# Optimization experiments

Hardware: AMD Instinct MI355X
Metric: run time of the kernel (lower is better)

## Reference

```python
import jax, jax.numpy as jnp
from jax import lax
import numpy as np

D_MODEL = 512
D_INNER = 1024   # expand=2 * d_model
D_STATE = 16
D_CONV = 4
DT_RANK = 32     # ceil(d_model/16)
B_SZ = 2
SEQ = 8192


def setup_inputs() -> dict:
    key = jax.random.key(0)
    ks = jax.random.split(key, 20)
    def n(k, shape, s=0.02):
        return jax.random.normal(k, shape, jnp.float32) * s
    inp = {
        "hidden_states": jax.random.normal(ks[0], (B_SZ, SEQ, D_MODEL), jnp.float32),
        "in_proj_w": n(ks[1], (2 * D_INNER, D_MODEL)),
        "out_proj_w": n(ks[2], (D_MODEL, D_INNER)),
    }
    for i, sfx in enumerate(["f", "r"]):
        b = 3 + i * 7
        inp[f"conv_w_{sfx}"] = n(ks[b], (D_INNER, 1, D_CONV), 0.1)
        inp[f"conv_b_{sfx}"] = n(ks[b + 1], (D_INNER,), 0.1)
        inp[f"xproj_w_{sfx}"] = n(ks[b + 2], (DT_RANK + 2 * D_STATE, D_INNER))
        inp[f"dtproj_w_{sfx}"] = n(ks[b + 3], (D_INNER, DT_RANK), 0.1)
        # softplus-inverse of dt_init ~0.01 (Mamba-style dt bias init)
        inp[f"dtproj_b_{sfx}"] = jnp.log(jnp.expm1(jnp.full((D_INNER,), 0.01, jnp.float32)))
        inp[f"A_log_{sfx}"] = jnp.log(jnp.tile(jnp.arange(1, D_STATE + 1, dtype=jnp.float32), (D_INNER, 1)))
        inp[f"D_{sfx}"] = jnp.ones((D_INNER,), jnp.float32)
    return inp


def _mamba(u, in_w, out_w, conv_w, conv_b, xproj_w, dt_w, dt_b, A_log, D_skip):
    # u: (B, L, D_MODEL)
    B, L, _ = u.shape
    xz = jnp.einsum('bld,ed->ble', u, in_w)          # (B, L, 2*D_INNER)
    x, z = jnp.split(xz, 2, axis=-1)
    # depthwise causal conv1d over time
    xt = lax.conv_general_dilated(
        x.transpose(0, 2, 1), conv_w, (1,), [(D_CONV - 1, 0)],
        dimension_numbers=('NCH', 'OIH', 'NCH'), feature_group_count=D_INNER)
    x = jax.nn.silu(xt.transpose(0, 2, 1) + conv_b)   # (B, L, D_INNER)
    # input-dependent dt, B, C
    xdbl = jnp.einsum('ble,fe->blf', x, xproj_w)      # (B, L, DT_RANK + 2*D_STATE)
    dt = xdbl[..., :DT_RANK]
    Bm = xdbl[..., DT_RANK:DT_RANK + D_STATE]         # (B, L, N)
    Cm = xdbl[..., DT_RANK + D_STATE:]                # (B, L, N)
    delta = jax.nn.softplus(jnp.einsum('blr,er->ble', dt, dt_w) + dt_b)  # (B, L, D_INNER)
    A = -jnp.exp(A_log)                               # (D_INNER, N)
    dA = jnp.exp(delta[..., None] * A)                # (B, L, D_INNER, N)
    dBu = delta[..., None] * Bm[:, :, None, :] * x[..., None]

    def step(h, inps):
        dA_t, dBu_t, C_t = inps
        h = dA_t * h + dBu_t                          # (B, D_INNER, N)
        return h, jnp.einsum('ben,bn->be', h, C_t)

    h0 = jnp.zeros((B, D_INNER, D_STATE), u.dtype)
    _, ys = lax.scan(step, h0, (dA.transpose(1, 0, 2, 3),
                                dBu.transpose(1, 0, 2, 3),
                                Cm.transpose(1, 0, 2)))
    y = ys.transpose(1, 0, 2) + x * D_skip            # (B, L, D_INNER)
    y = y * jax.nn.silu(z)
    return jnp.einsum('ble,de->bld', y, out_w)


def reference(hidden_states, in_proj_w, out_proj_w,
              conv_w_f, conv_b_f, xproj_w_f, dtproj_w_f, dtproj_b_f, A_log_f, D_f,
              conv_w_r, conv_b_r, xproj_w_r, dtproj_w_r, dtproj_b_r, A_log_r, D_r):
    out = _mamba(hidden_states, in_proj_w, out_proj_w,
                 conv_w_f, conv_b_f, xproj_w_f, dtproj_w_f, dtproj_b_f, A_log_f, D_f)
    out_rev = _mamba(hidden_states[:, ::-1], in_proj_w, out_proj_w,
                     conv_w_r, conv_b_r, xproj_w_r, dtproj_w_r, dtproj_b_r, A_log_r, D_r)[:, ::-1]
    return out + out_rev
```

## Files before the change

kernel.cpp:

```cpp
#include <hip/hip_runtime.h>
#include <hip/hip_bf16.h>
#include <math.h>

#define B_SZ 2
#define SEQ  8192
#define DM   512
#define DI   1024
#define DS   16
#define DTR  32
#define M_TOT (B_SZ*SEQ)
#define LOG2E 1.44269504088896f
#define NCHAN  (4*DI*DS)
#define NG     (4*DI)

typedef __attribute__((ext_vector_type(8))) short bf16x8;
typedef __attribute__((ext_vector_type(4))) float f32x4;
typedef unsigned short u16;

struct TrueT  { static constexpr bool value = true;  };
struct FalseT { static constexpr bool value = false; };

__device__ __forceinline__ float bf2f(u16 u){
  union { unsigned u; float f; } v; v.u = ((unsigned)u) << 16; return v.f;
}
__device__ __forceinline__ u16 f2bf(float f){
  union { float f; unsigned u; } v; v.f = f;
  unsigned r = v.u + 0x7FFFu + ((v.u >> 16) & 1u);
  return (u16)(r >> 16);
}
__device__ __forceinline__ float silu_f(float x){ return x / (1.f + __expf(-x)); }
__device__ __forceinline__ float softplus_f(float x){
  return (x > 15.f) ? x : __logf(1.f + __expf(x));
}

template<bool S>
__device__ __forceinline__ void dA_calc(float d, const float* A2, float A20, float* dAv){
  if (S) {
    const float q = exp2f(A20 * d);
    dAv[0]  = q;
    dAv[1]  = q * q;
    dAv[2]  = dAv[1] * q;
    dAv[3]  = dAv[1] * dAv[1];
    dAv[4]  = dAv[3] * q;
    dAv[5]  = dAv[3] * dAv[1];
    dAv[6]  = dAv[3] * dAv[2];
    dAv[7]  = dAv[3] * dAv[3];
    dAv[8]  = dAv[7] * q;
    dAv[9]  = dAv[7] * dAv[1];
    dAv[10] = dAv[7] * dAv[2];
    dAv[11] = dAv[7] * dAv[3];
    dAv[12] = dAv[7] * dAv[4];
    dAv[13] = dAv[7] * dAv[5];
    dAv[14] = dAv[7] * dAv[6];
    dAv[15] = dAv[7] * dAv[7];
  } else {
    #pragma unroll
    for (int n = 0; n < DS; n++) dAv[n] = exp2f(A2[n] * d);
  }
}

__global__ __launch_bounds__(256) void cvt_k(
    const float* __restrict__ s, u16* __restrict__ d)
{
  const size_t i = (size_t)blockIdx.x * 256 + threadIdx.x;
  const float4 a = ((const float4*)s)[i * 2];
  const float4 b = ((const float4*)s)[i * 2 + 1];
  union { uint4 v; u16 h[8]; } o;
  o.h[0] = f2bf(a.x); o.h[1] = f2bf(a.y); o.h[2] = f2bf(a.z); o.h[3] = f2bf(a.w);
  o.h[4] = f2bf(b.x); o.h[5] = f2bf(b.y); o.h[6] = f2bf(b.z); o.h[7] = f2bf(b.w);
  ((uint4*)d)[i] = o.v;
}

#define WU_INW  131072
#define WU_XW   8192
#define WU_DTW  4096
#define WU_OUTW 65536
#define WU_TOT  (WU_INW + 2*WU_XW + 2*WU_DTW + WU_OUTW)
__global__ __launch_bounds__(256) void cvtw_k(
    const float* __restrict__ inw, const float* __restrict__ xwf,
    const float* __restrict__ xwr, const float* __restrict__ dtwf,
    const float* __restrict__ dtwr, const float* __restrict__ outw,
    u16* __restrict__ dst)
{
  int i = blockIdx.x * 256 + threadIdx.x;
  const float* s;
  int base = 0;
  if (i < WU_INW) { s = inw; }
  else if ((i -= WU_INW) < WU_XW) { s = xwf; base = WU_INW; }
  else if ((i -= WU_XW) < WU_XW)  { s = xwr; base = WU_INW + WU_XW; }
  else if ((i -= WU_XW) < WU_DTW) { s = dtwf; base = WU_INW + 2*WU_XW; }
  else if ((i -= WU_DTW) < WU_DTW){ s = dtwr; base = WU_INW + 2*WU_XW + WU_DTW; }
  else { i -= WU_DTW; s = outw; base = WU_INW + 2*WU_XW + 2*WU_DTW; }
  const float4 a = ((const float4*)s)[i * 2];
  const float4 b = ((const float4*)s)[i * 2 + 1];
  union { uint4 v; u16 h[8]; } o;
  o.h[0] = f2bf(a.x); o.h[1] = f2bf(a.y); o.h[2] = f2bf(a.z); o.h[3] = f2bf(a.w);
  o.h[4] = f2bf(b.x); o.h[5] = f2bf(b.y); o.h[6] = f2bf(b.z); o.h[7] = f2bf(b.w);
  ((uint4*)(dst))[base + i] = o.v;
}

template<int BN, int EPI, bool DUAL>
__global__ __launch_bounds__(256) void gemm_k(
    const u16* __restrict__ Ap,  const u16* __restrict__ Ap2, int lda,
    const u16* __restrict__ Bw,  const u16* __restrict__ Bw2, int K,
    void* __restrict__ out0, void* __restrict__ out02,
    void* __restrict__ out1,
    const float* __restrict__ bias, const float* __restrict__ bias2, int ldo)
{
  constexpr int BM = 128, BK = 32;
  __shared__ __align__(16) u16 As[BM * BK];
  __shared__ __align__(16) u16 Bs[BN * BK];
  const int tid  = threadIdx.x;
  const int lane = tid & 63, wid = tid >> 6;
  const int mt = blockIdx.x, nt = blockIdx.y;
  const int z  = DUAL ? blockIdx.z : 0;
  const u16* A = z ? Ap2 : Ap;
  const u16* W = z ? Bw2 : Bw;
  void* o0 = z ? out02 : out0;
  const float* bi = z ? bias2 : bias;

  constexpr int FM = (BN == 128) ? 4 : 2;
  const int wm = (BN == 128) ? ((wid >> 1) * 64) : (wid * 32);
  const int wn = (BN == 128) ? ((wid & 1) * 64) : 0;

  f32x4 acc[FM][4];
  #pragma unroll
  for (int i = 0; i < FM; i++)
    #pragma unroll
    for (int j = 0; j < 4; j++)
      acc[i][j] = (f32x4){0.f, 0.f, 0.f, 0.f};

  const int sr = lane >> 2;
  const int sc = (lane & 3) * 8;

  for (int k0 = 0; k0 < K; k0 += BK) {
    #pragma unroll
    for (int j = 0; j < 2; j++) {
      const int chunk = wid * 2 + j;
      const u16* src = A + (size_t)(mt * BM + chunk * 16 + sr) * lda + (k0 + sc);
      __builtin_amdgcn_global_load_lds(
          (const __attribute__((address_space(1))) void*)src,
          (__attribute__((address_space(3))) void*)(As + chunk * 512), 16, 0, 0);
    }
    #pragma unroll
    for (int j = 0; j < BN / 64; j++) {
      const int chunk = wid * (BN / 64) + j;
      const u16* src = W + (size_t)(nt * BN + chunk * 16 + sr) * K + (k0 + sc);
      __builtin_amdgcn_global_load_lds(
          (const __attribute__((address_space(1))) void*)src,
          (__attribute__((address_space(3))) void*)(Bs + chunk * 512), 16, 0, 0);
    }
    __syncthreads();

    const int row = lane & 15, kq = (lane >> 4) * 8;
    bf16x8 af[FM], bfr[4];
    #pragma unroll
    for (int i = 0; i < FM; i++) af[i] = *(const bf16x8*)&As[(wm + i * 16 + row) * BK + kq];
    #pragma unroll
    for (int j = 0; j < 4; j++)  bfr[j] = *(const bf16x8*)&Bs[(wn + j * 16 + row) * BK + kq];
    #pragma unroll
    for (int i = 0; i < FM; i++)
      #pragma unroll
      for (int j = 0; j < 4; j++)
        acc[i][j] = __builtin_amdgcn_mfma_f32_16x16x32_bf16(af[i], bfr[j], acc[i][j], 0, 0, 0);
    __syncthreads();
  }

  const int rb4 = (lane >> 4) * 4, col = lane & 15;
  #pragma unroll
  for (int i = 0; i < FM; i++) {
    #pragma unroll
    for (int j = 0; j < 4; j++) {
      #pragma unroll
      for (int r = 0; r < 4; r++) {
        const int m = mt * BM + wm + i * 16 + rb4 + r;
        const int n = nt * BN + wn + j * 16 + col;
        const float v = acc[i][j][r];
        if (EPI == 0) {
          if (n < DI) ((u16*)o0)[(size_t)m * DI + n] = f2bf(v);
          else        ((u16*)out1)[(size_t)m * DI + (n - DI)] = f2bf(silu_f(v));
        } else if (EPI == 1) {
          ((u16*)o0)[(size_t)m * ldo + n] = f2bf(v);
        } else if (EPI == 2) {
          ((u16*)o0)[(size_t)m * ldo + n] = f2bf(softplus_f(v + bi[n]));
        } else {
          ((float*)o0)[(size_t)m * ldo + n] = v;
        }
      }
    }
  }
}

__global__ __launch_bounds__(256) void conv_k(
    const u16* __restrict__ xpre,
    const float* __restrict__ wf, const float* __restrict__ bf_,
    const float* __restrict__ wr, const float* __restrict__ br_,
    u16* __restrict__ xf, u16* __restrict__ xr)
{
  const int lt  = blockIdx.x;
  const int b   = blockIdx.y & 1;
  const int dir = blockIdx.y >> 1;
  const int tid = threadIdx.x;
  const float* w  = dir ? wr : wf;
  const float* bb = dir ? br_ : bf_;
  u16* xo = dir ? xr : xf;
  const int l0 = lt * 64;
  for (int j = 0; j < 4; j++) {
    const int e = j * 256 + tid;
    const float w0 = w[e*4+0], w1 = w[e*4+1], w2 = w[e*4+2], w3 = w[e*4+3], bv = bb[e];
    const size_t base = (size_t)b * SEQ * DI + e;
    auto load = [&](int q) -> float {
      if (q < 0) return 0.f;
      const int li = dir ? (SEQ - 1 - q) : q;
      return bf2f(xpre[base + (size_t)li * DI]);
    };
    float h0 = load(l0 - 3), h1 = load(l0 - 2), h2 = load(l0 - 1);
    for (int l = l0; l < l0 + 64; l++) {
      const float h3 = load(l);
      const float v = bv + w0*h0 + w1*h1 + w2*h2 + w3*h3;
      xo[base + (size_t)l * DI] = f2bf(silu_f(v));
      h0 = h1; h1 = h2; h2 = h3;
    }
  }
}

template<bool PRE>
__global__ __launch_bounds__(256) void scanA_k(
    const u16* __restrict__ xdblf_, const u16* __restrict__ xdblr_,
    const u16* __restrict__ xf_,    const u16* __restrict__ xr_,
    const float* __restrict__ Alf,  const float* __restrict__ Alr,
    const float* __restrict__ dtwf, const float* __restrict__ dtwr,
    const float* __restrict__ dtbf, const float* __restrict__ dtbr,
    const u16* __restrict__ df_,    const u16* __restrict__ dr_,
    float* __restrict__ sumdP, float* __restrict__ bP, int ct)
{
  const int e = blockIdx.x * 256 + threadIdx.x;
  const int c = blockIdx.y;
  const int dir = blockIdx.z >> 1, b = blockIdx.z & 1;
  const u16* xdbl = dir ? xdblr_ : xdblf_;
  const u16* x    = dir ? xr_ : xf_;
  const float* Al = dir ? Alr : Alf;
  const u16* dpre = dir ? dr_ : df_;

  float A2[DS], h[DS], dw[DTR];
  #pragma unroll
  for (int n = 0; n < DS; n++) { A2[n] = -__expf(Al[e * DS + n]) * LOG2E; h[n] = 0.f; }
  const float A20 = A2[0];
  bool structured = true;
  #pragma unroll
  for (int n = 1; n < DS; n++)
    structured = structured && (fabsf(A2[n] - (float)(n + 1) * A20) <= 1e-3f * fabsf(A2[n]));

  float bias = 0.f;
  if (!PRE) {
    const float* dtw = dir ? dtwr : dtwf;
    #pragma unroll
    for (int r = 0; r < DTR; r += 4) {
      const float4 v = *(const float4*)(dtw + e * DTR + r);
      dw[r] = v.x; dw[r+1] = v.y; dw[r+2] = v.z; dw[r+3] = v.w;
    }
    bias = (dir ? dtbr : dtbf)[e];
  }

  float sumd = 0.f;
  const size_t m0 = (size_t)b * SEQ + (size_t)c * ct;

  auto core = [&](auto sc) {
    constexpr bool S = decltype(sc)::value;
    for (int t = 0; t < ct; t++) {
      const size_t m = m0 + t;
      float d;
      if (PRE) {
        d = bf2f(dpre[m * DI + e]);
      } else {
        union { uint4 v[4]; u16 s[32]; } DT;
        #pragma unroll
        for (int q = 0; q < 4; q++) DT.v[q] = ((const uint4*)(xdbl + m * 64))[q];
        float a0 = 0.f, a1 = 0.f, a2 = 0.f, a3 = 0.f;
        #pragma unroll
        for (int r = 0; r < DTR; r += 4) {
          a0 += bf2f(DT.s[r+0]) * dw[r+0];
          a1 += bf2f(DT.s[r+1]) * dw[r+1];
          a2 += bf2f(DT.s[r+2]) * dw[r+2];
          a3 += bf2f(DT.s[r+3]) * dw[r+3];
        }
        d = softplus_f(((a0 + a1) + (a2 + a3)) + bias);
      }
      const float xv  = bf2f(x[m * DI + e]);
      const float dbx = d * xv;
      sumd += d;
      union { uint4 v[2]; u16 s[16]; } Bv;
      Bv.v[0] = ((const uint4*)(xdbl + m * 64 + 32))[0];
      Bv.v[1] = ((const uint4*)(xdbl + m * 64 + 32))[1];
      float dAv[DS];
      dA_calc<S>(d, A2, A20, dAv);
      #pragma unroll
      for (int n = 0; n < DS; n++)
        h[n] = dAv[n] * h[n] + dbx * bf2f(Bv.s[n]);
    }
  };
  if (structured) core(TrueT{}); else core(FalseT{});

  const int g = (dir * 2 + b) * DI + e;
  const size_t cb = (size_t)c * NCHAN + (size_t)g * DS;
  #pragma unroll
  for (int n = 0; n < DS; n++) bP[cb + n] = h[n];
  sumdP[(size_t)c * NG + g] = sumd;
}

__global__ __launch_bounds__(256) void scanB_k(
    const float* __restrict__ sumdP, float* __restrict__ bP,
    const float* __restrict__ Alog_f, const float* __restrict__ Alog_r, int nchunk)
{
  const int ch = blockIdx.x * 256 + threadIdx.x;
  const int g = ch >> 4, n = ch & 15;
  const int dir = g >> 11, e = g & (DI - 1);
  const float* Al = dir ? Alog_r : Alog_f;
  const float A2 = -__expf(Al[e * DS + n]) * LOG2E;
  float h = 0.f;
  for (int c = 0; c < nchunk; c++) {
    const float a = exp2f(A2 * sumdP[(size_t)c * NG + g]);
    const size_t i = (size_t)c * NCHAN + ch;
    const float bb = bP[i];
    bP[i] = h;
    h = a * h + bb;
  }
}

template<bool PRE, int MODE>
__global__ __launch_bounds__(256) void scanC_k(
    const u16* __restrict__ xdblf_, const u16* __restrict__ xdblr_,
    const u16* __restrict__ xf_,    const u16* __restrict__ xr_,
    const float* __restrict__ Alf,  const float* __restrict__ Alr,
    const float* __restrict__ dtwf, const float* __restrict__ dtwr,
    const float* __restrict__ dtbf, const float* __restrict__ dtbr,
    const u16* __restrict__ df_,    const u16* __restrict__ dr_,
    const float* __restrict__ Dskf, const float* __restrict__ Dskr,
    const float* __restrict__ hin,
    u16* __restrict__ yf, u16* __restrict__ yr,
    const u16* __restrict__ szp, int ct)
{
  const int e = blockIdx.x * 256 + threadIdx.x;
  const int c = blockIdx.y;
  int dir, b;
  if (MODE == 0) { dir = blockIdx.z >> 1; b = blockIdx.z & 1; }
  else           { dir = (MODE == 2);     b = blockIdx.z; }
  const u16* xdbl = dir ? xdblr_ : xdblf_;
  const u16* x    = dir ? xr_ : xf_;
  const float* Al = dir ? Alr : Alf;
  const u16* dpre = dir ? dr_ : df_;
  const float dskip = (dir ? Dskr : Dskf)[e];

  float A2[DS], h[DS], dw[DTR];
  #pragma unroll
  for (int n = 0; n < DS; n++) A2[n] = -__expf(Al[e * DS + n]) * LOG2E;
  const float A20 = A2[0];
  bool structured = true;
  #pragma unroll
  for (int n = 1; n < DS; n++)
    structured = structured && (fabsf(A2[n] - (float)(n + 1) * A20) <= 1e-3f * fabsf(A2[n]));

  float bias = 0.f;
  if (!PRE) {
    const float* dtw = dir ? dtwr : dtwf;
    #pragma unroll
    for (int r = 0; r < DTR; r += 4) {
      const float4 v = *(const float4*)(dtw + e * DTR + r);
      dw[r] = v.x; dw[r+1] = v.y; dw[r+2] = v.z; dw[r+3] = v.w;
    }
    bias = (dir ? dtbr : dtbf)[e];
  }

  const int g = (dir * 2 + b) * DI + e;
  const size_t cb = (size_t)c * NCHAN + (size_t)g * DS;
  #pragma unroll
  for (int n = 0; n < DS; n++) h[n] = hin[cb + n];
  const size_t m0 = (size_t)b * SEQ + (size_t)c * ct;

  auto core = [&](auto sc) {
    constexpr bool S = decltype(sc)::value;
    for (int t = 0; t < ct; t++) {
      const size_t m = m0 + t;
      float d;
      union { uint4 v[4]; u16 s[32]; } BC;
      #pragma unroll
      for (int q = 0; q < 4; q++) BC.v[q] = ((const uint4*)(xdbl + m * 64 + 32))[q];
      if (PRE) {
        d = bf2f(dpre[m * DI + e]);
      } else {
        union { uint4 v[4]; u16 s[32]; } DT;
        #pragma unroll
        for (int q = 0; q < 4; q++) DT.v[q] = ((const uint4*)(xdbl + m * 64))[q];
        float a0 = 0.f, a1 = 0.f, a2 = 0.f, a3 = 0.f;
        #pragma unroll
        for (int r = 0; r < DTR; r += 4) {
          a0 += bf2f(DT.s[r+0]) * dw[r+0];
          a1 += bf2f(DT.s[r+1]) * dw[r+1];
          a2 += bf2f(DT.s[r+2]) * dw[r+2];
          a3 += bf2f(DT.s[r+3]) * dw[r+3];
        }
        d = softplus_f(((a0 + a1) + (a2 + a3)) + bias);
      }
      const float xv  = bf2f(x[m * DI + e]);
      const float dbx = d * xv;
      float dAv[DS];
      dA_calc<S>(d, A2, A20, dAv);
      float y = 0.f;
      #pragma unroll
      for (int n = 0; n < DS; n++) {
        h[n] = dAv[n] * h[n] + dbx * bf2f(BC.s[n]);
        y += h[n] * bf2f(BC.s[16 + n]);
      }
      const float yout = y + xv * dskip;
      if (MODE == 0) {
        if (dir == 0) {
          yf[m * DI + e] = f2bf(yout);
        } else {
          const size_t mo = (size_t)b * SEQ + (SEQ - 1 - (c * ct + t));
          yr[mo * DI + e] = f2bf(yout);
        }
      } else if (MODE == 1) {
        yf[m * DI + e] = f2bf(yout);
      } else {
        const size_t mo = (size_t)b * SEQ + (SEQ - 1 - (c * ct + t));
        const size_t moi = mo * DI + e;
        yr[moi] = f2bf((bf2f(yf[moi]) + yout) * bf2f(szp[moi]));
      }
    }
  };
  if (structured) core(TrueT{}); else core(FalseT{});
}

__global__ __launch_bounds__(256) void comb_k(
    u16* __restrict__ yfp, const u16* __restrict__ yrp, const u16* __restrict__ szp)
{
  const size_t i = ((size_t)blockIdx.x * 256 + threadIdx.x) * 8;
  union { uint4 v; u16 s[8]; } A, Bq, S, O;
  A.v  = *(const uint4*)(yfp + i);
  Bq.v = *(const uint4*)(yrp + i);
  S.v  = *(const uint4*)(szp + i);
  #pragma unroll
  for (int j = 0; j < 8; j++)
    O.s[j] = f2bf((bf2f(A.s[j]) + bf2f(Bq.s[j])) * bf2f(S.s[j]));
  *(uint4*)(yfp + i) = O.v;
}

extern "C" void kernel_launch(void* const* d_in, const int* in_sizes, int n_in,
                              void* d_out, int out_size, void* d_ws, size_t ws_size,
                              hipStream_t stream)
{
  (void)in_sizes; (void)n_in; (void)out_size;
  const float* u      = (const float*)d_in[0];
  const float* in_w   = (const float*)d_in[1];
  const float* out_w  = (const float*)d_in[2];
  const float* cw_f   = (const float*)d_in[3];
  const float* cb_f   = (const float*)d_in[4];
  const float* xw_f   = (const float*)d_in[5];
  const float* dtw_f  = (const float*)d_in[6];
  const float* dtb_f  = (const float*)d_in[7];
  const float* Alog_f = (const float*)d_in[8];
  const float* D_f    = (const float*)d_in[9];
  const float* cw_r   = (const float*)d_in[10];
  const float* cb_r   = (const float*)d_in[11];
  const float* xw_r   = (const float*)d_in[12];
  const float* dtw_r  = (const float*)d_in[13];
  const float* dtb_r  = (const float*)d_in[14];
  const float* Alog_r = (const float*)d_in[15];
  const float* D_r    = (const float*)d_in[16];

  const size_t mexe = (size_t)M_TOT * DI;
  const size_t need_big =
      5 * (mexe * 2) + 2 * ((size_t)M_TOT * 64 * 2) + (size_t)WU_TOT * 16 +
      (size_t)128 * NG * 4 + (size_t)128 * NCHAN * 4 + 32 * 256;
  const bool big = (ws_size >= need_big);
  const int nchunk = big ? 128 : 64;
  const int ct = SEQ / nchunk;

  char* ws = (char*)d_ws;
  size_t off = 0;
  auto alloc = [&](size_t bytes) -> void* {
    void* p = ws + off;
    off += (bytes + 255) & ~(size_t)255;
    return p;
  };
  u16*   ubf   = (u16*)alloc(mexe * 2);
  u16*   xpre  = (u16*)alloc(mexe * 2);
  u16*   xf    = (u16*)alloc(mexe * 2);
  u16*   xr    = (u16*)alloc(mexe * 2);
  u16*   xdblf = (u16*)alloc((size_t)M_TOT * 64 * 2);
  u16*   xdblr = (u16*)alloc((size_t)M_TOT * 64 * 2);
  u16*   wbf   = (u16*)alloc((size_t)WU_TOT * 16);
  float* sumdP = (float*)alloc((size_t)nchunk * NG * 4);
  float* bP    = (float*)alloc((size_t)nchunk * NCHAN * 4);
  u16*   dr    = big ? (u16*)alloc(mexe * 2) : nullptr;
  u16*   df    = ubf;
  u16*   szb   = (u16*)d_out;

  u16* winb  = wbf;
  u16* xwbf  = wbf + (size_t)WU_INW * 8;
  u16* xwbr  = xwbf + (size_t)WU_XW * 8;
  u16* dtwbf = xwbr + (size_t)WU_XW * 8;
  u16* dtwbr = dtwbf + (size_t)WU_DTW * 8;
  u16* outwb = dtwbr + (size_t)WU_DTW * 8;

  dim3 blk(256);
  cvt_k<<<dim3((unsigned)((size_t)M_TOT * DM / 8 / 256)), blk, 0, stream>>>(u, ubf);
  cvtw_k<<<dim3(WU_TOT / 256), blk, 0, stream>>>(in_w, xw_f, xw_r, dtw_f, dtw_r, out_w, wbf);
  gemm_k<128, 0, false><<<dim3(128, 16), blk, 0, stream>>>(
      ubf, nullptr, DM, winb, nullptr, DM, xpre, nullptr, szb, nullptr, nullptr, 0);
  conv_k<<<dim3(128, 4), blk, 0, stream>>>(xpre, cw_f, cb_f, cw_r, cb_r, xf, xr);
  gemm_k<64, 1, true><<<dim3(128, 1, 2), blk, 0, stream>>>(
      xf, xr, DI, xwbf, xwbr, DI, xdblf, xdblr, nullptr, nullptr, nullptr, 64);

  if (big) {
    gemm_k<128, 2, true><<<dim3(128, 8, 2), blk, 0, stream>>>(
        xdblf, xdblr, 64, dtwbf, dtwbr, DTR, df, dr, nullptr, dtb_f, dtb_r, DI);
    scanA_k<true><<<dim3(4, nchunk, 4), blk, 0, stream>>>(
        xdblf, xdblr, xf, xr, Alog_f, Alog_r, dtw_f, dtw_r, dtb_f, dtb_r,
        df, dr, sumdP, bP, ct);
    scanB_k<<<dim3(NCHAN / 256), blk, 0, stream>>>(sumdP, bP, Alog_f, Alog_r, nchunk);
    scanC_k<true, 0><<<dim3(4, nchunk, 4), blk, 0, stream>>>(
        xdblf, xdblr, xf, xr, Alog_f, Alog_r, dtw_f, dtw_r, dtb_f, dtb_r,
        df, dr, D_f, D_r, bP, xf, xpre, nullptr, ct);
    comb_k<<<dim3((unsigned)(mexe / 8 / 256)), blk, 0, stream>>>(xf, xpre, szb);
    gemm_k<128, 3, false><<<dim3(128, 4), blk, 0, stream>>>(
        xf, nullptr, DI, outwb, nullptr, DI, d_out, nullptr, nullptr, nullptr, nullptr, DM);
  } else {
    scanA_k<false><<<dim3(4, nchunk, 4), blk, 0, stream>>>(
        xdblf, xdblr, xf, xr, Alog_f, Alog_r, dtw_f, dtw_r, dtb_f, dtb_r,
        nullptr, nullptr, sumdP, bP, ct);
    scanB_k<<<dim3(NCHAN / 256), blk, 0, stream>>>(sumdP, bP, Alog_f, Alog_r, nchunk);
    scanC_k<false, 1><<<dim3(4, nchunk, 2), blk, 0, stream>>>(
        xdblf, xdblr, xf, xr, Alog_f, Alog_r, dtw_f, dtw_r, dtb_f, dtb_r,
        nullptr, nullptr, D_f, D_r, bP, xf, nullptr, nullptr, ct);
    scanC_k<false, 2><<<dim3(4, nchunk, 2), blk, 0, stream>>>(
        xdblf, xdblr, xf, xr, Alog_f, Alog_r, dtw_f, dtw_r, dtb_f, dtb_r,
        nullptr, nullptr, D_f, D_r, bP, xf, xpre, szb, ct);
    gemm_k<128, 3, false><<<dim3(128, 4), blk, 0, stream>>>(
        xpre, nullptr, DI, outwb, nullptr, DI, d_out, nullptr, nullptr, nullptr, nullptr, DM);
  }
}
```

Measured before the change: 437.0 us.

## Rewrite depthwise conv with vectorized loads and fused forward/reverse passes

Replaces the depthwise causal conv kernel with one where each thread handles 8 contiguous channels through 128-bit loads and stores. Both the forward and the reverse direction are computed from a single read of the pre-activation input, and the reverse output is written to its flipped position. The grid becomes many small 8-step time tiles instead of 64-step tiles. This aims to halve input reads and cut the narrow 2-byte memory transactions of the old kernel, in exchange for a few redundant halo loads per tile and more registers per thread.

Result: faster. 374.5 us (-14.3%).

```diff
diff --git a/kernel.cpp b/kernel.cpp
--- a/kernel.cpp
+++ b/kernel.cpp
@@ -12,6 +12,7 @@
 #define LOG2E 1.44269504088896f
 #define NCHAN  (4*DI*DS)
 #define NG     (4*DI)
+#define CLT    8
 
 typedef __attribute__((ext_vector_type(8))) short bf16x8;
 typedef __attribute__((ext_vector_type(4))) float f32x4;
@@ -191,36 +192,72 @@
   }
 }
 
-__global__ __launch_bounds__(256) void conv_k(
+__global__ __launch_bounds__(256) void conv2_k(
     const u16* __restrict__ xpre,
     const float* __restrict__ wf, const float* __restrict__ bf_,
     const float* __restrict__ wr, const float* __restrict__ br_,
     u16* __restrict__ xf, u16* __restrict__ xr)
 {
-  const int lt  = blockIdx.x;
-  const int b   = blockIdx.y & 1;
-  const int dir = blockIdx.y >> 1;
-  const int tid = threadIdx.x;
-  const float* w  = dir ? wr : wf;
-  const float* bb = dir ? br_ : bf_;
-  u16* xo = dir ? xr : xf;
-  const int l0 = lt * 64;
-  for (int j = 0; j < 4; j++) {
-    const int e = j * 256 + tid;
-    const float w0 = w[e*4+0], w1 = w[e*4+1], w2 = w[e*4+2], w3 = w[e*4+3], bv = bb[e];
-    const size_t base = (size_t)b * SEQ * DI + e;
-    auto load = [&](int q) -> float {
-      if (q < 0) return 0.f;
-      const int li = dir ? (SEQ - 1 - q) : q;
-      return bf2f(xpre[base + (size_t)li * DI]);
-    };
-    float h0 = load(l0 - 3), h1 = load(l0 - 2), h2 = load(l0 - 1);
-    for (int l = l0; l < l0 + 64; l++) {
-      const float h3 = load(l);
-      const float v = bv + w0*h0 + w1*h1 + w2*h2 + w3*h3;
-      xo[base + (size_t)l * DI] = f2bf(silu_f(v));
-      h0 = h1; h1 = h2; h2 = h3;
-    }
+  const int tid  = threadIdx.x;
+  const int et   = tid & 127;
+  const int lsub = tid >> 7;
+  const int e0 = et * 8;
+  const int b  = blockIdx.y;
+  const int l0 = (blockIdx.x * 2 + lsub) * CLT;
+  const size_t base = (size_t)b * SEQ * DI + e0;
+
+  float4 wf4[8], wr4[8];
+  float  bfv[8], brv[8];
+  #pragma unroll
+  for (int j = 0; j < 8; j++) {
+    wf4[j] = *(const float4*)(wf + (e0 + j) * 4);
+    wr4[j] = *(const float4*)(wr + (e0 + j) * 4);
+    bfv[j] = bf_[e0 + j];
+    brv[j] = br_[e0 + j];
+  }
+
+  float c0[8], c1[8], c2[8];
+  auto loadv = [&](int l, float* dst) {
+    if (l < 0 || l >= SEQ) {
+      #pragma unroll
+      for (int j = 0; j < 8; j++) dst[j] = 0.f;
+      return;
+    }
+    union { uint4 v; u16 s[8]; } t;
+    t.v = *(const uint4*)(xpre + base + (size_t)l * DI);
+    #pragma unroll
+    for (int j = 0; j < 8; j++) dst[j] = bf2f(t.s[j]);
+  };
+  loadv(l0 - 3, c0); loadv(l0 - 2, c1); loadv(l0 - 1, c2);
+
+  #pragma unroll
+  for (int i = 0; i < CLT + 3; i++) {
+    const int l = l0 + i;
+    float cn[8];
+    loadv(l, cn);
+    if (i < CLT) {
+      union { uint4 v; u16 s[8]; } o;
+      #pragma unroll
+      for (int j = 0; j < 8; j++) {
+        const float v = bfv[j] + wf4[j].x * c0[j] + wf4[j].y * c1[j]
+                               + wf4[j].z * c2[j] + wf4[j].w * cn[j];
+        o.s[j] = f2bf(silu_f(v));
+      }
+      *(uint4*)(xf + base + (size_t)l * DI) = o.v;
+    }
+    if (i >= 3) {
+      const int lr = l - 3;
+      union { uint4 v; u16 s[8]; } o;
+      #pragma unroll
+      for (int j = 0; j < 8; j++) {
+        const float v = brv[j] + wr4[j].w * c0[j] + wr4[j].z * c1[j]
+                               + wr4[j].y * c2[j] + wr4[j].x * cn[j];
+        o.s[j] = f2bf(silu_f(v));
+      }
+      *(uint4*)(xr + base + (size_t)(SEQ - 1 - lr) * DI) = o.v;
+    }
+    #pragma unroll
+    for (int j = 0; j < 8; j++) { c0[j] = c1[j]; c1[j] = c2[j]; c2[j] = cn[j]; }
   }
 }
 
@@ -508,7 +545,8 @@
   cvtw_k<<<dim3(WU_TOT / 256), blk, 0, stream>>>(in_w, xw_f, xw_r, dtw_f, dtw_r, out_w, wbf);
   gemm_k<128, 0, false><<<dim3(128, 16), blk, 0, stream>>>(
       ubf, nullptr, DM, winb, nullptr, DM, xpre, nullptr, szb, nullptr, nullptr, 0);
-  conv_k<<<dim3(128, 4), blk, 0, stream>>>(xpre, cw_f, cb_f, cw_r, cb_r, xf, xr);
+  conv2_k<<<dim3(SEQ / (2 * CLT), B_SZ), blk, 0, stream>>>(
+      xpre, cw_f, cb_f, cw_r, cb_r, xf, xr);
   gemm_k<64, 1, true><<<dim3(128, 1, 2), blk, 0, stream>>>(
       xf, xr, DI, xwbf, xwbr, DI, xdblf, xdblr, nullptr, nullptr, nullptr, 64);
 
```
